# Kernel optimization log

Hardware: AMD Instinct MI355X
Metric: run time of the kernel (lower is better)

The kernel has to match this reference:

```python
import jax, jax.numpy as jnp
import numpy as np

K = 16          # neighbours
H = 4           # attention heads
EPS = 1e-5      # batchnorm eps


def setup_inputs() -> dict:
    key = jax.random.key(0)
    ks = jax.random.split(key, 12)
    N, P, D, Cin = 8, 2048, 3, 64
    chans = [64, 64, 128]
    edge_in = 2 * Cin
    Cout = chans[-1]
    hid = Cout // 4       # se_ratio=4
    ah = 32               # attn_hidden

    def w(k, shape, fan):
        return jax.random.normal(k, shape, jnp.float32) / np.float32(np.sqrt(fan))

    return {
        "points": jax.random.normal(ks[0], (N, P, D), jnp.float32),
        "features": jax.random.normal(ks[1], (N, P, Cin), jnp.float32),
        "conv_w0": w(ks[2], (chans[0], edge_in), edge_in),
        "conv_w1": w(ks[3], (chans[1], chans[0]), chans[0]),
        "conv_w2": w(ks[4], (chans[2], chans[1]), chans[1]),
        "bn_g0": jnp.ones(chans[0], jnp.float32), "bn_b0": jnp.zeros(chans[0], jnp.float32),
        "bn_g1": jnp.ones(chans[1], jnp.float32), "bn_b1": jnp.zeros(chans[1], jnp.float32),
        "bn_g2": jnp.ones(chans[2], jnp.float32), "bn_b2": jnp.zeros(chans[2], jnp.float32),
        "attn_w1": w(ks[5], (ah, edge_in), edge_in),
        "attn_b1": jnp.zeros(ah, jnp.float32),
        "attn_w2": w(ks[6], (H, ah), ah),
        "attn_b2": jnp.zeros(H, jnp.float32),
        "tau": jnp.ones((1,), jnp.float32),
        "sc_w": w(ks[7], (Cout, Cin), Cin),
        "sc_g": jnp.ones(Cout, jnp.float32), "sc_b": jnp.zeros(Cout, jnp.float32),
        "se_w1": w(ks[8], (hid, Cout), Cout),
        "se_w2": w(ks[9], (Cout, hid), hid),
    }


def _bn(x, g, b, axes):
    # training-mode batch norm over `axes`, channels-last
    mu = x.mean(axes, keepdims=True)
    var = x.var(axes, keepdims=True)
    return (x - mu) * jax.lax.rsqrt(var + EPS) * g + b


def reference(points, features, conv_w0, conv_w1, conv_w2,
              bn_g0, bn_b0, bn_g1, bn_b1, bn_g2, bn_b2,
              attn_w1, attn_b1, attn_w2, attn_b2, tau,
              sc_w, sc_g, sc_b, se_w1, se_w2):
    N, P, Cin = features.shape
    # pairwise squared distances (N,P,P)
    r = jnp.sum(points * points, axis=-1)
    dist = r[:, :, None] - 2.0 * jnp.einsum('npd,nqd->npq', points, points) + r[:, None, :]
    _, idx = jax.lax.top_k(-dist, K + 1)
    idx = idx[:, :, 1:]                                # drop self, (N,P,K)

    nbr = jax.vmap(lambda f, i: f[i])(features, idx)   # (N,P,K,Cin)
    center = features[:, :, None, :]
    edge = jnp.concatenate([jnp.broadcast_to(center, nbr.shape), nbr - center], axis=-1)  # (N,P,K,2Cin)

    # GAT-style attention weights over K
    a = jnp.einsum('npke,he->npkh', edge, attn_w1) + attn_b1
    a = jax.nn.leaky_relu(a, 0.2)
    a = jnp.einsum('npkh,oh->npko', a, attn_w2) + attn_b2   # (N,P,K,H)
    w = jax.nn.softmax(a / tau[0], axis=2)

    # edge MLP (1x1 convs) + BN(train) + ReLU
    x = edge
    for wm, g, b in ((conv_w0, bn_g0, bn_b0), (conv_w1, bn_g1, bn_b1), (conv_w2, bn_g2, bn_b2)):
        x = jnp.einsum('npkc,oc->npko', x, wm)
        x = jax.nn.relu(_bn(x, g, b, (0, 1, 2)))

    # multi-head attention pooling over K
    C = x.shape[-1]
    x = x.reshape(N, P, K, H, C // H)
    x = jnp.einsum('npkhd,npkh->nphd', x, w).reshape(N, P, C)

    # SE gate
    s = jax.nn.sigmoid(jax.nn.relu(x.mean(axis=1) @ se_w1.T) @ se_w2.T)  # (N,C)
    x = x * s[:, None, :]

    # shortcut branch
    sc = jnp.einsum('npc,oc->npo', features, sc_w)
    sc = jax.nn.relu(_bn(sc, sc_g, sc_b, (0, 1)))
    return x + sc
```

## Files before the change

kernel.cpp:

```cpp
#include <hip/hip_runtime.h>
#include <hip/hip_bf16.h>

#define N_   8
#define P_   2048
#define K_   16
#define T1   8

typedef const float* fpp;
typedef __attribute__((ext_vector_type(8))) short short8;
typedef __attribute__((ext_vector_type(4))) short short4v;
typedef __attribute__((ext_vector_type(4))) float floatx4;

__device__ __forceinline__ float bcast(float v, int lane){
    return __uint_as_float(__builtin_amdgcn_readlane(__float_as_uint(v), (unsigned)lane));
}
__device__ __forceinline__ short f2bf(float f){
    unsigned u = __float_as_uint(f);
    unsigned r = (u + 0x7FFFu + ((u >> 16) & 1u)) >> 16;
    return (short)r;
}
__device__ __forceinline__ float bf2f(short s){
    return __uint_as_float(((unsigned)(unsigned short)s) << 16);
}
__device__ __forceinline__ float bf2fu(unsigned short s){
    return __uint_as_float(((unsigned)s) << 16);
}

__global__ __launch_bounds__(256) void pts_prep_kernel(fpp points, float4* pts4){
    const int i = blockIdx.x*256 + threadIdx.x;
    const float x = points[i*3+0], y = points[i*3+1], z = points[i*3+2];
    pts4[i] = make_float4(x, y, z, x*x + y*y + z*z);
}

__global__ __launch_bounds__(256) void knn_kernel(const float4* pts4, int* idxo){
    const int t = threadIdx.x;
    const int wave = t >> 6, lane = t & 63;
    const int n  = blockIdx.x >> 8;
    const int p0 = (blockIdx.x & 255) * 8;
    const int base = n << 11;
    const float4* cand = pts4 + base;
    const int plb = p0 + wave*2;
    float px[2], py[2], pz[2], rp[2];
    #pragma unroll
    for (int i=0;i<2;i++){
        const float4 me = cand[plb + i];
        px[i]=me.x; py[i]=me.y; pz[i]=me.z; rp[i]=me.w;
    }
    float sd[2]; int sq[2];
    {
        const float4 c = cand[lane];
        #pragma unroll
        for (int i=0;i<2;i++){
            sd[i] = (rp[i] - 2.0f*(px[i]*c.x + py[i]*c.y + pz[i]*c.z)) + c.w;
            sq[i] = lane;
        }
        #pragma unroll
        for (int k = 2; k <= 64; k <<= 1){
            #pragma unroll
            for (int j = k >> 1; j > 0; j >>= 1){
                const bool takeSmaller = ((lane & k) == 0) == ((lane & j) == 0);
                #pragma unroll
                for (int i=0;i<2;i++){
                    const float od = __shfl_xor(sd[i], j);
                    const int   oi = __shfl_xor(sq[i], j);
                    const bool otherLess = (od < sd[i]) || (od == sd[i] && oi < sq[i]);
                    const bool take = (takeSmaller == otherLess);
                    sd[i] = take ? od : sd[i];
                    sq[i] = take ? oi : sq[i];
                }
            }
        }
    }
    for (int s = 1; s < 32; ++s){
        const int ci0 = s*64;
        const float4 c = cand[ci0 + lane];
        float d[2]; unsigned long long mask[2];
        #pragma unroll
        for (int i=0;i<2;i++)
            d[i] = (rp[i] - 2.0f*(px[i]*c.x + py[i]*c.y + pz[i]*c.z)) + c.w;
        #pragma unroll
        for (int i=0;i<2;i++){
            const float thr = bcast(sd[i], 16);
            mask[i] = __ballot(d[i] < thr);
        }
        while (mask[0] | mask[1]){
            #pragma unroll
            for (int i=0;i<2;i++){
                if (mask[i]){
                    const int src = __ffsll((long long)mask[i]) - 1;
                    mask[i] &= mask[i] - 1;
                    const float dn = bcast(d[i], src);
                    const int   qn = ci0 + src;
                    float shd = __shfl_up(sd[i], 1);
                    int   shq = __shfl_up(sq[i], 1);
                    if (lane == 0) shd = -__builtin_inff();
                    const bool c1 = shd > dn;
                    const bool c2 = sd[i] > dn;
                    sq[i] = c1 ? shq : (c2 ? qn : sq[i]);
                    sd[i] = c1 ? shd : (c2 ? dn : sd[i]);
                }
            }
        }
    }
    if (lane >= 1 && lane <= 16){
        #pragma unroll
        for (int i=0;i<2;i++)
            idxo[(base + plb + i)*K_ + (lane - 1)] = base + sq[i];
    }
}

__global__ __launch_bounds__(192) void feat_gemm_kernel(fpp feat, fpp w0, fpp aw1,
        float* U, float* V, float* AU, float* AV){
    const int t = threadIdx.x;
    const int w = t >> 6, lane = t & 63;
    const int row0 = blockIdx.x * 16;
    float wreg[64];
    if (w == 0){
        #pragma unroll
        for (int c=0;c<64;c++) wreg[c] = w0[lane*128+c] - w0[lane*128+64+c];
    } else if (w == 1){
        #pragma unroll
        for (int c=0;c<64;c++) wreg[c] = w0[lane*128+64+c];
    } else {
        if (lane < 32){
            #pragma unroll
            for (int c=0;c<64;c++) wreg[c] = aw1[lane*128+c] - aw1[lane*128+64+c];
        } else {
            const int o = lane - 32;
            #pragma unroll
            for (int c=0;c<64;c++) wreg[c] = aw1[o*128+64+c];
        }
    }
    for (int r=0;r<16;r++){
        const int row = row0 + r;
        const float fv = feat[row*64 + lane];
        float acc = 0.f;
        #pragma unroll
        for (int c=0;c<64;c++) acc = fmaf(bcast(fv, c), wreg[c], acc);
        if      (w==0) U[row*64+lane]=acc;
        else if (w==1) V[row*64+lane]=acc;
        else { if (lane<32) AU[row*32+lane]=acc; else AV[row*32+lane-32]=acc; }
    }
}

__global__ __launch_bounds__(128) void sc_stats_kernel(fpp feat, fpp scw, float* scs, float* scq){
    __shared__ float swc[128*65];
    __shared__ float sf[64*64];
    const int t = threadIdx.x;
    for (int i=t;i<8192;i+=128) swc[(i>>6)*65+(i&63)] = scw[i];
    const int row0 = blockIdx.x*64;
    for (int i=t;i<4096;i+=128) sf[i] = feat[row0*64+i];
    __syncthreads();
    float psum=0.f, psq=0.f;
    for (int r=0;r<64;r++){
        float acc = 0.f;
        #pragma unroll
        for (int k=0;k<64;k++) acc = fmaf(sf[r*64+k], swc[t*65+k], acc);
        psum += acc; psq += acc*acc;
    }
    atomicAdd(&scs[t], psum);
    atomicAdd(&scq[t], psq);
}

__global__ __launch_bounds__(256) void attn_bn0_kernel(const int* idx, const float* U, const float* V,
        const float* AU, const float* AV, fpp b1, fpp w2, fpp b2, fpp tau,
        float* attw, float* bn0s, float* bn0q){
    __shared__ float sAV[4][16][36];
    const int t = threadIdx.x, w = t>>6, lane = t&63;
    const int pt0 = blockIdx.x*32 + w*8;
    const int kk = lane >> 2, h = lane & 3;
    float w2r[32];
    #pragma unroll
    for (int c=0;c<32;c++) w2r[c] = w2[h*32+c];
    const float b2v = b2[h];
    const float tv  = tau[0];
    float ssum=0.f, ssq=0.f;
    for (int j=0;j<8;j++){
        const int pt = pt0 + j;
        const int* ip = idx + pt*K_;
        {
            const int fl = lane >> 2, part = lane & 3;
            const int qf = ip[fl];
            const float4 a = *(const float4*)&AV[qf*32 + part*8];
            const float4 b = *(const float4*)&AV[qf*32 + part*8 + 4];
            *(float4*)&sAV[w][fl][part*8]     = a;
            *(float4*)&sAV[w][fl][part*8 + 4] = b;
        }
        __builtin_amdgcn_wave_barrier();
        const float uv = U[pt*64+lane];
        for (int k=0;k<K_;k++){
            const int q = ip[k];
            const float v = uv + V[q*64+lane];
            ssum += v; ssq += v*v;
        }
        float a2 = b2v;
        for (int c=0;c<32;c++){
            float a1 = AU[pt*32+c] + sAV[w][kk][c] + b1[c];
            a1 = a1 > 0.f ? a1 : 0.2f*a1;
            a2 = fmaf(a1, w2r[c], a2);
        }
        const float lt = a2 / tv;
        float m = lt;
        m = fmaxf(m, __shfl_xor(m, 4));  m = fmaxf(m, __shfl_xor(m, 8));
        m = fmaxf(m, __shfl_xor(m, 16)); m = fmaxf(m, __shfl_xor(m, 32));
        const float e = expf(lt - m);
        float s = e;
        s += __shfl_xor(s, 4);  s += __shfl_xor(s, 8);
        s += __shfl_xor(s, 16); s += __shfl_xor(s, 32);
        attw[pt*64 + lane] = e / s;
        __builtin_amdgcn_wave_barrier();
    }
    __shared__ float rs[256], rq[256];
    rs[t]=ssum; rq[t]=ssq; __syncthreads();
    if (t < 64){
        atomicAdd(&bn0s[t], rs[t]+rs[t+64]+rs[t+128]+rs[t+192]);
        atomicAdd(&bn0q[t], rq[t]+rq[t+64]+rq[t+128]+rq[t+192]);
    }
}

__global__ __launch_bounds__(128) void bn_finalize_kernel(const float* s, const float* q, fpp g, fpp b,
        float inv_cnt, int C, float* scale, float* shift){
    const int c = threadIdx.x;
    if (c < C){
        const float mu  = s[c]*inv_cnt;
        const float var = fmaxf(q[c]*inv_cnt - mu*mu, 0.f);
        const float sc  = g[c] * rsqrtf(var + 1e-5f);
        scale[c]=sc; shift[c] = b[c] - mu*sc;
    }
}

__global__ __launch_bounds__(192) void bn_finalize2_kernel(const float* s0, const float* q0,
        fpp g0, fpp b0, const float* ss, const float* qs, fpp gs, fpp bs,
        float* sc0, float* sh0, float* scsc, float* shsc){
    const int c = threadIdx.x;
    if (c < 64){
        const float mu  = s0[c]*(1.0f/262144.0f);
        const float var = fmaxf(q0[c]*(1.0f/262144.0f) - mu*mu, 0.f);
        const float sc  = g0[c] * rsqrtf(var + 1e-5f);
        sc0[c]=sc; sh0[c]=b0[c]-mu*sc;
    } else {
        const int cc = c - 64;
        const float mu  = ss[cc]*(1.0f/16384.0f);
        const float var = fmaxf(qs[cc]*(1.0f/16384.0f) - mu*mu, 0.f);
        const float sc  = gs[cc] * rsqrtf(var + 1e-5f);
        scsc[cc]=sc; shsc[cc]=bs[cc]-mu*sc;
    }
}

__global__ __launch_bounds__(512) void mfma_conv1_kernel(const int* idx, const float* U, const float* V,
        fpp w1, const float* sc0, const float* sh0, float* bn1s, float* bn1q,
        unsigned short* y1out){
    __shared__ __align__(16) short WH[64*72], WL[64*72];
    __shared__ __align__(16) short AH[64*72], AL[64*72];
    __shared__ float ssum[64], ssq[64];
    const int t = threadIdx.x, lane = t & 63, w = t >> 6;
    const int L = lane & 15, Q = lane >> 4;
    for (int i = t; i < 4096; i += 512){
        const float wv = w1[i];
        const short hh = f2bf(wv);
        const int n = i >> 6, k = i & 63;
        WH[n*72+k] = hh;
        WL[n*72+k] = f2bf(wv - bf2f(hh));
    }
    if (t < 64){ ssum[t]=0.f; ssq[t]=0.f; }
    __syncthreads();
    const int nbase = (w >> 2) * 2;
    short8 bh[2][2], bl[2][2];
    #pragma unroll
    for (int nt=0; nt<2; ++nt){
        #pragma unroll
        for (int ks=0; ks<2; ++ks){
            const int off = ((nbase+nt)*16+L)*72 + ks*32 + Q*8;
            bh[nt][ks] = *(const short8*)&WH[off];
            bl[nt][ks] = *(const short8*)&WL[off];
        }
    }
    const int m0 = (w & 3) * 16;
    const int r = t >> 3, c8 = (t & 7) * 8;
    float sacc[2] = {0,0}, qacc[2] = {0,0};
    for (int tile = 0; tile < T1; ++tile){
        __syncthreads();
        const int e0 = (blockIdx.x*T1 + tile) * 64;
        {
            const int s = e0 + r;
            const int p = s >> 4, q = idx[s];
            const float4* up = (const float4*)&U[p*64 + c8];
            const float4* vq = (const float4*)&V[q*64 + c8];
            #pragma unroll
            for (int b4=0; b4<2; ++b4){
                const float4 uv4 = up[b4];
                const float4 vv4 = vq[b4];
                const int c0 = c8 + b4*4;
                float av[4] = {uv4.x+vv4.x, uv4.y+vv4.y, uv4.z+vv4.z, uv4.w+vv4.w};
                short4v h4, l4;
                #pragma unroll
                for (int j=0;j<4;j++){
                    const int c = c0 + j;
                    const float a0 = fmaxf(fmaf(av[j], sc0[c], sh0[c]), 0.f);
                    const short hh = f2bf(a0);
                    h4[j] = hh;
                    l4[j] = f2bf(a0 - bf2f(hh));
                }
                *(short4v*)&AH[r*72 + c0] = h4;
                *(short4v*)&AL[r*72 + c0] = l4;
            }
        }
        __syncthreads();
        floatx4 acc[2];
        #pragma unroll
        for (int nt=0;nt<2;nt++) acc[nt] = (floatx4){0.f,0.f,0.f,0.f};
        #pragma unroll
        for (int ks=0; ks<2; ++ks){
            const int aoff = (m0 + L)*72 + ks*32 + Q*8;
            const short8 ah = *(const short8*)&AH[aoff];
            const short8 al = *(const short8*)&AL[aoff];
            #pragma unroll
            for (int nt=0;nt<2;nt++){
                acc[nt] = __builtin_amdgcn_mfma_f32_16x16x32_bf16(ah, bh[nt][ks], acc[nt], 0,0,0);
                acc[nt] = __builtin_amdgcn_mfma_f32_16x16x32_bf16(ah, bl[nt][ks], acc[nt], 0,0,0);
                acc[nt] = __builtin_amdgcn_mfma_f32_16x16x32_bf16(al, bh[nt][ks], acc[nt], 0,0,0);
            }
        }
        #pragma unroll
        for (int nt=0;nt<2;nt++){
            const int o = (nbase+nt)*16 + L;
            #pragma unroll
            for (int rr=0;rr<4;rr++){
                const float v = acc[nt][rr];
                y1out[(e0 + m0 + Q*4 + rr)*64 + o] = (unsigned short)f2bf(v);
                sacc[nt]+=v; qacc[nt]+=v*v;
            }
        }
    }
    #pragma unroll
    for (int nt=0;nt<2;nt++){
        atomicAdd(&ssum[(nbase+nt)*16+L], sacc[nt]);
        atomicAdd(&ssq [(nbase+nt)*16+L], qacc[nt]);
    }
    __syncthreads();
    if (t < 64){
        atomicAdd(&bn1s[t], ssum[t]);
        atomicAdd(&bn1q[t], ssq[t]);
    }
}

__global__ __launch_bounds__(512) void mfma_conv2_kernel(const unsigned short* y1in,
        fpp w2, const float* sc1, const float* sh1,
        float* bn2s, float* bn2q, unsigned short* y2out){
    __shared__ __align__(16) short WH2[128*72], WL2[128*72];
    __shared__ __align__(16) short AH[64*72], AL[64*72];
    __shared__ float ssum[128], ssq[128];
    const int t = threadIdx.x, lane = t & 63, w = t >> 6;
    const int L = lane & 15, Q = lane >> 4;
    for (int i = t; i < 8192; i += 512){
        const float wv = w2[i];
        const short hh = f2bf(wv);
        WH2[(i>>6)*72+(i&63)] = hh;
        WL2[(i>>6)*72+(i&63)] = f2bf(wv - bf2f(hh));
    }
    if (t < 128){ ssum[t]=0.f; ssq[t]=0.f; }
    const int nbase = (w >> 2) * 4;
    const int m0 = (w & 3) * 16;
    const int r = t >> 3, c8 = (t & 7) * 8;
    float s1r[8], h1r[8];
    #pragma unroll
    for (int j=0;j<8;j++){ s1r[j] = sc1[c8+j]; h1r[j] = sh1[c8+j]; }
    float sacc[4] = {0,0,0,0}, qacc[4] = {0,0,0,0};
    for (int tile = 0; tile < T1; ++tile){
        __syncthreads();
        const int e0 = (blockIdx.x*T1 + tile) * 64;
        {
            const short8 y8 = *(const short8*)&y1in[(e0 + r)*64 + c8];
            short4v h4, l4;
            #pragma unroll
            for (int g=0; g<2; ++g){
                #pragma unroll
                for (int j=0;j<4;j++){
                    const int jj = g*4 + j;
                    const float a1 = fmaxf(fmaf(bf2fu((unsigned short)y8[jj]),
                                                s1r[jj], h1r[jj]), 0.f);
                    const short hh = f2bf(a1);
                    h4[j] = hh;
                    l4[j] = f2bf(a1 - bf2f(hh));
                }
                const int c0 = c8 + g*4;
                *(short4v*)&AH[r*72 + c0] = h4;
                *(short4v*)&AL[r*72 + c0] = l4;
            }
        }
        __syncthreads();
        floatx4 acc2[4];
        #pragma unroll
        for (int nt=0;nt<4;nt++) acc2[nt] = (floatx4){0.f,0.f,0.f,0.f};
        #pragma unroll
        for (int ks=0; ks<2; ++ks){
            const int aoff = (m0 + L)*72 + ks*32 + Q*8;
            const short8 ah = *(const short8*)&AH[aoff];
            const short8 al = *(const short8*)&AL[aoff];
            #pragma unroll
            for (int nt=0;nt<4;nt++){
                const int boff = ((nbase+nt)*16+L)*72 + ks*32 + Q*8;
                const short8 wh = *(const short8*)&WH2[boff];
                const short8 wl = *(const short8*)&WL2[boff];
                acc2[nt] = __builtin_amdgcn_mfma_f32_16x16x32_bf16(ah, wh, acc2[nt], 0,0,0);
                acc2[nt] = __builtin_amdgcn_mfma_f32_16x16x32_bf16(ah, wl, acc2[nt], 0,0,0);
                acc2[nt] = __builtin_amdgcn_mfma_f32_16x16x32_bf16(al, wh, acc2[nt], 0,0,0);
            }
        }
        #pragma unroll
        for (int nt=0;nt<4;nt++){
            const int o = (nbase+nt)*16 + L;
            #pragma unroll
            for (int rr=0;rr<4;rr++){
                const float v = acc2[nt][rr];
                const int s = e0 + m0 + Q*4 + rr;
                y2out[s*128 + o] = (unsigned short)f2bf(v);
                sacc[nt] += v; qacc[nt] += v*v;
            }
        }
    }
    #pragma unroll
    for (int nt=0;nt<4;nt++){
        atomicAdd(&ssum[(nbase+nt)*16+L], sacc[nt]);
        atomicAdd(&ssq [(nbase+nt)*16+L], qacc[nt]);
    }
    __syncthreads();
    if (t < 128){
        atomicAdd(&bn2s[t], ssum[t]);
        atomicAdd(&bn2q[t], ssq[t]);
    }
}

__global__ __launch_bounds__(256) void combine_fast_kernel(const unsigned short* y2, const float* attw,
        const float* sc2, const float* sh2, float* xcomb, float* msum){
    __shared__ float rs[512];
    const int t=threadIdx.x, w=t>>6, lane=t&63;
    const float s2a=sc2[lane], h2a=sh2[lane], s2b=sc2[64+lane], h2b=sh2[64+lane];
    const int pt0 = blockIdx.x*16 + w*4;
    const int hsel = lane >> 5;
    float m0=0.f, m1=0.f;
    for (int j=0;j<4;j++){
        const int pt = pt0 + j;
        float acc0=0.f, acc1=0.f;
        for (int k=0;k<K_;k++){
            const int s = pt*K_ + k;
            const float r0 = fmaxf(fmaf(bf2fu(y2[s*128+lane]),    s2a, h2a), 0.f);
            const float r1 = fmaxf(fmaf(bf2fu(y2[s*128+64+lane]), s2b, h2b), 0.f);
            acc0 = fmaf(r0, attw[s*4 + hsel],     acc0);
            acc1 = fmaf(r1, attw[s*4 + 2 + hsel], acc1);
        }
        xcomb[pt*128+lane]    = acc0;
        xcomb[pt*128+64+lane] = acc1;
        m0 += acc0; m1 += acc1;
    }
    rs[t]=m0; rs[256+t]=m1; __syncthreads();
    if (t<64){
        const int n = (blockIdx.x*16) >> 11;
        atomicAdd(&msum[n*128+t],    rs[t]+rs[t+64]+rs[t+128]+rs[t+192]);
        atomicAdd(&msum[n*128+64+t], rs[256+t]+rs[256+t+64]+rs[256+t+128]+rs[256+t+192]);
    }
}

__global__ __launch_bounds__(128) void se_kernel(const float* msum, fpp w1se, fpp w2se, float* sev){
    __shared__ float tl[32];
    const int t = threadIdx.x;
    for (int n=0;n<N_;n++){
        if (t < 32){
            float acc=0.f;
            for (int c=0;c<128;c++) acc = fmaf(msum[n*128+c]*(1.f/2048.f), w1se[t*128+c], acc);
            tl[t] = fmaxf(acc, 0.f);
        }
        __syncthreads();
        float acc=0.f;
        for (int hh=0;hh<32;hh++) acc = fmaf(tl[hh], w2se[t*32+hh], acc);
        sev[n*128+t] = 1.f/(1.f+expf(-acc));
        __syncthreads();
    }
}

__global__ __launch_bounds__(128) void final_kernel(fpp feat, fpp scw, const float* xcomb,
        const float* sev, const float* scsc, const float* shsc, float* out){
    __shared__ float swc[128*65];
    __shared__ float sf[64*64];
    const int t = threadIdx.x;
    for (int i=t;i<8192;i+=128) swc[(i>>6)*65+(i&63)] = scw[i];
    const int row0 = blockIdx.x*64;
    for (int i=t;i<4096;i+=128) sf[i] = feat[row0*64+i];
    __syncthreads();
    const int c = t;
    const float scl = scsc[c], shf = shsc[c];
    for (int r=0;r<64;r++){
        const int row = row0 + r;
        float acc = 0.f;
        #pragma unroll
        for (int k=0;k<64;k++) acc = fmaf(sf[r*64+k], swc[c*65+k], acc);
        const int n = row >> 11;
        out[row*128+c] = xcomb[row*128+c]*sev[n*128+c] + fmaxf(fmaf(acc, scl, shf), 0.f);
    }
}

extern "C" void kernel_launch(void* const* d_in, const int* in_sizes, int n_in,
                              void* d_out, int out_size, void* d_ws, size_t ws_size,
                              hipStream_t stream) {
    fpp points  = (fpp)d_in[0];
    fpp feat    = (fpp)d_in[1];
    fpp conv_w0 = (fpp)d_in[2];
    fpp conv_w1 = (fpp)d_in[3];
    fpp conv_w2 = (fpp)d_in[4];
    fpp bn_g0 = (fpp)d_in[5],  bn_b0 = (fpp)d_in[6];
    fpp bn_g1 = (fpp)d_in[7],  bn_b1 = (fpp)d_in[8];
    fpp bn_g2 = (fpp)d_in[9],  bn_b2 = (fpp)d_in[10];
    fpp attn_w1 = (fpp)d_in[11], attn_b1 = (fpp)d_in[12];
    fpp attn_w2 = (fpp)d_in[13], attn_b2 = (fpp)d_in[14];
    fpp tau  = (fpp)d_in[15];
    fpp sc_w = (fpp)d_in[16], sc_g = (fpp)d_in[17], sc_b = (fpp)d_in[18];
    fpp se_w1 = (fpp)d_in[19], se_w2 = (fpp)d_in[20];

    float* W = (float*)d_ws;
    float* BN0S=W+0;    float* BN0Q=W+64;
    float* BN1S=W+128;  float* BN1Q=W+192;
    float* BN2S=W+256;  float* BN2Q=W+384;
    float* SCS =W+512;  float* SCQ =W+640;
    float* SC0 =W+768;  float* SH0 =W+832;
    float* SC1 =W+896;  float* SH1 =W+960;
    float* SC2 =W+1024; float* SH2 =W+1152;
    float* SCSC=W+1280; float* SHSC=W+1408;
    float* MSUM=W+1536; float* SEV =W+2560;
    int*   IDX  = (int*)(W + 4096);
    float* U    = W + 266240;
    float* V    = U + 1048576;
    float* AU   = V + 1048576;
    float* AV   = AU + 524288;
    float* ATTW = AV + 524288;
    float* XCOMB= ATTW + 1048576;
    unsigned short* Y2 = (unsigned short*)(W + 6557696);
    unsigned short* Y1 = Y2 + 33554432;
    float4* PTS4 = (float4*)XCOMB;

    hipMemsetAsync(d_ws, 0, 4096*sizeof(float), stream);

    pts_prep_kernel<<<64, 256, 0, stream>>>(points, PTS4);
    knn_kernel<<<2048, 256, 0, stream>>>(PTS4, IDX);
    feat_gemm_kernel<<<1024, 192, 0, stream>>>(feat, conv_w0, attn_w1, U, V, AU, AV);
    sc_stats_kernel<<<256, 128, 0, stream>>>(feat, sc_w, SCS, SCQ);
    attn_bn0_kernel<<<512, 256, 0, stream>>>(IDX, U, V, AU, AV,
                                             attn_b1, attn_w2, attn_b2, tau,
                                             ATTW, BN0S, BN0Q);
    bn_finalize2_kernel<<<1, 192, 0, stream>>>(BN0S, BN0Q, bn_g0, bn_b0,
                                               SCS, SCQ, sc_g, sc_b,
                                               SC0, SH0, SCSC, SHSC);
    mfma_conv1_kernel<<<512, 512, 0, stream>>>(IDX, U, V, conv_w1, SC0, SH0,
                                               BN1S, BN1Q, Y1);
    bn_finalize_kernel<<<1, 128, 0, stream>>>(BN1S, BN1Q, bn_g1, bn_b1,
                                              1.0f/262144.0f, 64, SC1, SH1);
    mfma_conv2_kernel<<<512, 512, 0, stream>>>(Y1, conv_w2, SC1, SH1,
                                               BN2S, BN2Q, Y2);
    bn_finalize_kernel<<<1, 128, 0, stream>>>(BN2S, BN2Q, bn_g2, bn_b2,
                                              1.0f/262144.0f, 128, SC2, SH2);
    combine_fast_kernel<<<1024, 256, 0, stream>>>(Y2, ATTW, SC2, SH2, XCOMB, MSUM);
    se_kernel<<<1, 128, 0, stream>>>(MSUM, se_w1, se_w2, SEV);
    final_kernel<<<256, 128, 0, stream>>>(feat, sc_w, XCOMB, SEV, SCSC, SHSC,
                                          (float*)d_out);
}
```

Baseline: 384.6 us.

## Fuse shortcut stats into feature GEMM, vectorize combine, split final kernel finer

Moves the shortcut-conv batch-norm statistics into feat_gemm_kernel by adding two extra wavefronts that hold sc_w rows, which removes the separate sc_stats kernel and its second pass over features. combine_fast_kernel now has each lane handle two adjacent bf16 channels with one 32-bit load and a float2 store, and shares one attention weight load between them. final_kernel is split from 256 blocks of 64 rows into 1024 blocks of 16 rows to use more of the GPU. The trade-offs are a larger block in the feature GEMM, many more atomics on the shortcut statistics (1024 blocks instead of 256), and the sc_w shared-memory staging now repeated four times as often in final_kernel.

```diff
diff --git a/kernel.cpp b/kernel.cpp
--- a/kernel.cpp
+++ b/kernel.cpp
@@ -109,8 +109,8 @@
     }
 }
 
-__global__ __launch_bounds__(192) void feat_gemm_kernel(fpp feat, fpp w0, fpp aw1,
-        float* U, float* V, float* AU, float* AV){
+__global__ __launch_bounds__(320) void feat_gemm_kernel(fpp feat, fpp w0, fpp aw1, fpp scw,
+        float* U, float* V, float* AU, float* AV, float* scs, float* scq){
     const int t = threadIdx.x;
     const int w = t >> 6, lane = t & 63;
     const int row0 = blockIdx.x * 16;
@@ -121,7 +121,7 @@
     } else if (w == 1){
         #pragma unroll
         for (int c=0;c<64;c++) wreg[c] = w0[lane*128+64+c];
-    } else {
+    } else if (w == 2){
         if (lane < 32){
             #pragma unroll
             for (int c=0;c<64;c++) wreg[c] = aw1[lane*128+c] - aw1[lane*128+64+c];
@@ -130,7 +130,12 @@
             #pragma unroll
             for (int c=0;c<64;c++) wreg[c] = aw1[o*128+64+c];
         }
-    }
+    } else {
+        const int o = (w-3)*64 + lane;
+        #pragma unroll
+        for (int c=0;c<64;c++) wreg[c] = scw[o*64+c];
+    }
+    float psum=0.f, psq=0.f;
     for (int r=0;r<16;r++){
         const int row = row0 + r;
         const float fv = feat[row*64 + lane];
@@ -139,27 +144,14 @@
         for (int c=0;c<64;c++) acc = fmaf(bcast(fv, c), wreg[c], acc);
         if      (w==0) U[row*64+lane]=acc;
         else if (w==1) V[row*64+lane]=acc;
-        else { if (lane<32) AU[row*32+lane]=acc; else AV[row*32+lane-32]=acc; }
-    }
-}
-
-__global__ __launch_bounds__(128) void sc_stats_kernel(fpp feat, fpp scw, float* scs, float* scq){
-    __shared__ float swc[128*65];
-    __shared__ float sf[64*64];
-    const int t = threadIdx.x;
-    for (int i=t;i<8192;i+=128) swc[(i>>6)*65+(i&63)] = scw[i];
-    const int row0 = blockIdx.x*64;
-    for (int i=t;i<4096;i+=128) sf[i] = feat[row0*64+i];
-    __syncthreads();
-    float psum=0.f, psq=0.f;
-    for (int r=0;r<64;r++){
-        float acc = 0.f;
-        #pragma unroll
-        for (int k=0;k<64;k++) acc = fmaf(sf[r*64+k], swc[t*65+k], acc);
-        psum += acc; psq += acc*acc;
-    }
-    atomicAdd(&scs[t], psum);
-    atomicAdd(&scq[t], psq);
+        else if (w==2){ if (lane<32) AU[row*32+lane]=acc; else AV[row*32+lane-32]=acc; }
+        else { psum += acc; psq += acc*acc; }
+    }
+    if (w >= 3){
+        const int o = (w-3)*64 + lane;
+        atomicAdd(&scs[o], psum);
+        atomicAdd(&scq[o], psq);
+    }
 }
 
 __global__ __launch_bounds__(256) void attn_bn0_kernel(const int* idx, const float* U, const float* V,
@@ -435,29 +427,31 @@
         const float* sc2, const float* sh2, float* xcomb, float* msum){
     __shared__ float rs[512];
     const int t=threadIdx.x, w=t>>6, lane=t&63;
-    const float s2a=sc2[lane], h2a=sh2[lane], s2b=sc2[64+lane], h2b=sh2[64+lane];
+    const int c0 = lane*2;
+    const float s2a=sc2[c0], h2a=sh2[c0], s2b=sc2[c0+1], h2b=sh2[c0+1];
     const int pt0 = blockIdx.x*16 + w*4;
-    const int hsel = lane >> 5;
+    const int hsel = lane >> 4;
     float m0=0.f, m1=0.f;
     for (int j=0;j<4;j++){
         const int pt = pt0 + j;
         float acc0=0.f, acc1=0.f;
         for (int k=0;k<K_;k++){
             const int s = pt*K_ + k;
-            const float r0 = fmaxf(fmaf(bf2fu(y2[s*128+lane]),    s2a, h2a), 0.f);
-            const float r1 = fmaxf(fmaf(bf2fu(y2[s*128+64+lane]), s2b, h2b), 0.f);
-            acc0 = fmaf(r0, attw[s*4 + hsel],     acc0);
-            acc1 = fmaf(r1, attw[s*4 + 2 + hsel], acc1);
-        }
-        xcomb[pt*128+lane]    = acc0;
-        xcomb[pt*128+64+lane] = acc1;
+            const unsigned v = *(const unsigned*)&y2[s*128 + c0];
+            const float aw = attw[s*4 + hsel];
+            const float r0 = fmaxf(fmaf(bf2fu((unsigned short)(v & 0xFFFFu)), s2a, h2a), 0.f);
+            const float r1 = fmaxf(fmaf(bf2fu((unsigned short)(v >> 16)),    s2b, h2b), 0.f);
+            acc0 = fmaf(r0, aw, acc0);
+            acc1 = fmaf(r1, aw, acc1);
+        }
+        *(float2*)&xcomb[pt*128 + c0] = make_float2(acc0, acc1);
         m0 += acc0; m1 += acc1;
     }
     rs[t]=m0; rs[256+t]=m1; __syncthreads();
     if (t<64){
         const int n = (blockIdx.x*16) >> 11;
-        atomicAdd(&msum[n*128+t],    rs[t]+rs[t+64]+rs[t+128]+rs[t+192]);
-        atomicAdd(&msum[n*128+64+t], rs[256+t]+rs[256+t+64]+rs[256+t+128]+rs[256+t+192]);
+        atomicAdd(&msum[n*128+2*t],   rs[t]+rs[t+64]+rs[t+128]+rs[t+192]);
+        atomicAdd(&msum[n*128+2*t+1], rs[256+t]+rs[256+t+64]+rs[256+t+128]+rs[256+t+192]);
     }
 }
 
@@ -481,15 +475,15 @@
 __global__ __launch_bounds__(128) void final_kernel(fpp feat, fpp scw, const float* xcomb,
         const float* sev, const float* scsc, const float* shsc, float* out){
     __shared__ float swc[128*65];
-    __shared__ float sf[64*64];
+    __shared__ float sf[16*64];
     const int t = threadIdx.x;
     for (int i=t;i<8192;i+=128) swc[(i>>6)*65+(i&63)] = scw[i];
-    const int row0 = blockIdx.x*64;
-    for (int i=t;i<4096;i+=128) sf[i] = feat[row0*64+i];
+    const int row0 = blockIdx.x*16;
+    for (int i=t;i<1024;i+=128) sf[i] = feat[row0*64+i];
     __syncthreads();
     const int c = t;
     const float scl = scsc[c], shf = shsc[c];
-    for (int r=0;r<64;r++){
+    for (int r=0;r<16;r++){
         const int row = row0 + r;
         float acc = 0.f;
         #pragma unroll
@@ -541,8 +535,8 @@
 
     pts_prep_kernel<<<64, 256, 0, stream>>>(points, PTS4);
     knn_kernel<<<2048, 256, 0, stream>>>(PTS4, IDX);
-    feat_gemm_kernel<<<1024, 192, 0, stream>>>(feat, conv_w0, attn_w1, U, V, AU, AV);
-    sc_stats_kernel<<<256, 128, 0, stream>>>(feat, sc_w, SCS, SCQ);
+    feat_gemm_kernel<<<1024, 320, 0, stream>>>(feat, conv_w0, attn_w1, sc_w,
+                                               U, V, AU, AV, SCS, SCQ);
     attn_bn0_kernel<<<512, 256, 0, stream>>>(IDX, U, V, AU, AV,
                                              attn_b1, attn_w2, attn_b2, tau,
                                              ATTW, BN0S, BN0Q);
@@ -559,6 +553,6 @@
                                               1.0f/262144.0f, 128, SC2, SH2);
     combine_fast_kernel<<<1024, 256, 0, stream>>>(Y2, ATTW, SC2, SH2, XCOMB, MSUM);
     se_kernel<<<1, 128, 0, stream>>>(MSUM, se_w1, se_w2, SEV);
-    final_kernel<<<256, 128, 0, stream>>>(feat, sc_w, XCOMB, SEV, SCSC, SHSC,
-                                          (float*)d_out);
-}
+    final_kernel<<<1024, 128, 0, stream>>>(feat, sc_w, XCOMB, SEV, SCSC, SHSC,
+                                           (float*)d_out);
+}
```

Result: no change. 379.8 us (-1.3%).
